# Kernel optimization log

Measured on AMD Instinct MI355X. Metric: run time of the kernel, lower is better.

The kernel has to match this reference:

```python
import jax, jax.numpy as jnp
import numpy as np

B, N, D = 256, 133, 1024
H, C = 8, 128  # per-head channels; H*C == out_channels
NEG_SLOPE = 0.2


def setup_inputs() -> dict:
    key = jax.random.key(0)
    kx, kw, ka, kadj = jax.random.split(key, 4)
    x = jax.random.normal(kx, (B, N, D), dtype=jnp.float32)
    W = jax.random.normal(kw, (H * C, D), dtype=jnp.float32) * 0.02  # nn.Linear weight (out,in)
    attn_w = jax.random.normal(ka, (2 * C,), dtype=jnp.float32) * 0.02  # attn Linear(2C,1) weight
    # binary adjacency with self-loops so every softmax column has a valid entry
    bern = (jax.random.uniform(kadj, (N, N)) < 0.15).astype(jnp.float32)
    adj = jnp.maximum(bern, jnp.eye(N, dtype=jnp.float32))[:, :, None]  # (N,N,1)
    return {"x": x, "W": W, "attn_w": attn_w, "adj": adj}


def reference(x, W, attn_w, adj):
    b, n, _ = x.shape
    g = (x @ W.T).reshape(b, n, H, C)  # (B,N,H,C)
    # concat(g_j, g_i) @ attn_w == g_j @ wl + g_i @ wr (leakyrelu applied after the sum)
    wl, wr = attn_w[:C], attn_w[C:]
    sj = jnp.einsum('bnhc,c->bnh', g, wl)  # score contribution from g[b, j]
    si = jnp.einsum('bnhc,c->bnh', g, wr)  # score contribution from g[b, i]
    e = jax.nn.leaky_relu(si[:, :, None, :] + sj[:, None, :, :], NEG_SLOPE)  # (B,N,N,H) e[b,i,j,h]
    e = jnp.where(adj[None] == 0, -jnp.inf, e)
    a = jax.nn.softmax(e, axis=1)  # faithful to original: softmax over dim=1 (the i axis)
    # dropout omitted (inference/eval mode)
    out = jnp.einsum('bijh,bjhf->bihf', a, g)  # aggregate over j
    return out.reshape(b, n, H * C)  # is_concat=True
```

## Files before the change

### kernel.cpp

```cpp
#include <hip/hip_runtime.h>

#define NB    133
#define NBP   136
#define BATCH 256
#define HEADS 8
#define CDIM  128
#define DDIM  1024
#define MROWS (BATCH * NB)
#define NDIM  (HEADS * CDIM)
#define BH    (BATCH * HEADS)
#define NT    32

typedef __bf16 bf16_t;
typedef bf16_t bf16x8 __attribute__((ext_vector_type(8)));
typedef float  f32x4  __attribute__((ext_vector_type(4)));

__device__ __forceinline__ unsigned short f2bf(float f) {
  unsigned u = __float_as_uint(f);
  u += 0x7fffu + ((u >> 16) & 1u);
  return (unsigned short)(u >> 16);
}
__device__ __forceinline__ void load_lds16(const void* g, void* l) {
  __builtin_amdgcn_global_load_lds(
      (__attribute__((address_space(1))) void*)(g),
      (__attribute__((address_space(3))) void*)(l), 16, 0, 0);
}
__device__ __forceinline__ void bar() {
  asm volatile("" ::: "memory");
  __builtin_amdgcn_s_barrier();
  asm volatile("" ::: "memory");
}
#define VMWAIT(n) asm volatile("s_waitcnt vmcnt(" #n ")" ::: "memory")

__global__ __launch_bounds__(256) void cvt_kernel(const float* __restrict__ x,
                                                  const float* __restrict__ W,
                                                  unsigned short* __restrict__ xb,
                                                  unsigned short* __restrict__ wb) {
  const int nx = MROWS * DDIM / 8, nw = NDIM * DDIM / 8;
  int i = blockIdx.x * 256 + threadIdx.x;
  const float* src; unsigned short* dst; int k;
  if (i < nx)           { src = x; dst = xb; k = i; }
  else if (i < nx + nw) { src = W; dst = wb; k = i - nx; }
  else return;
  const float4* s4 = (const float4*)src;
  float4 a = s4[(size_t)k * 2];
  float4 b = s4[(size_t)k * 2 + 1];
  union { unsigned short u[8]; uint4 v; } p;
  p.u[0] = f2bf(a.x); p.u[1] = f2bf(a.y); p.u[2] = f2bf(a.z); p.u[3] = f2bf(a.w);
  p.u[4] = f2bf(b.x); p.u[5] = f2bf(b.y); p.u[6] = f2bf(b.z); p.u[7] = f2bf(b.w);
  ((uint4*)dst)[k] = p.v;
}

__global__ __launch_bounds__(192) void mask_kernel(const float* __restrict__ adj,
                                                   unsigned* __restrict__ rm,
                                                   unsigned* __restrict__ cm) {
  const int tid = threadIdx.x, lane = tid & 63, wv = tid >> 6, blk = blockIdx.x;
  if (blk < 144) {
    const int i = blk;
    bool on = (i < NB) && (tid < NB) && (adj[i * NB + tid] != 0.f);
    unsigned long long bb = __ballot(on);
    if (lane == 0)  rm[i * 6 + wv * 2]     = (unsigned)bb;
    if (lane == 32) rm[i * 6 + wv * 2 + 1] = (unsigned)(bb >> 32);
  } else {
    const int j = blk - 144;
    bool on = (tid < NB) && (adj[tid * NB + j] != 0.f);
    unsigned long long bb = __ballot(on);
    if (lane == 0)  cm[j * 6 + wv * 2]     = (unsigned)bb;
    if (lane == 32) cm[j * 6 + wv * 2 + 1] = (unsigned)(bb >> 32);
  }
}

__global__ __launch_bounds__(512, 2) void gemm_kernel(const unsigned short* __restrict__ xb,
                                                      const unsigned short* __restrict__ wb,
                                                      const float* __restrict__ attn_w,
                                                      unsigned short* __restrict__ gb,
                                                      float* __restrict__ si_ws,
                                                      float* __restrict__ sj_ws) {
  __shared__ __attribute__((aligned(16))) unsigned short lds[4][2][8192];
  __shared__ float sred[2][8][128];

  const int tid = threadIdx.x;
  const int bn = blockIdx.x & 3, bm = blockIdx.x >> 2;
  const int lane = tid & 63, w = tid >> 6;
  const int wr = w >> 2, wc = w & 3;
  const int q = lane >> 4, li = lane & 15;
  const int sub = (q ^ ((li >> 1) & 3)) * 8;

  const unsigned short* Ab = xb + (size_t)bm * 256 * DDIM;
  const unsigned short* Bb = wb + (size_t)bn * 256 * DDIM;

  const int u0 = tid, u1 = tid + 512;
  const size_t sa0 = (size_t)(u0 >> 2) * DDIM + (((u0 & 3) ^ ((u0 >> 3) & 3)) * 8);
  const size_t sa1 = (size_t)(u1 >> 2) * DDIM + (((u1 & 3) ^ ((u1 >> 3) & 3)) * 8);

  f32x4 acc[8][4] = {};

#define STAGE(T) do { \
    unsigned short* _la = &lds[(T) & 3][0][0]; \
    unsigned short* _lb = &lds[(T) & 3][1][0]; \
    const int _k = (T) * 32; \
    load_lds16(Ab + sa0 + _k, _la + u0 * 8); \
    load_lds16(Ab + sa1 + _k, _la + u1 * 8); \
    load_lds16(Bb + sa0 + _k, _lb + u0 * 8); \
    load_lds16(Bb + sa1 + _k, _lb + u1 * 8); \
  } while (0)

#define COMPUTE(T) do { \
    const unsigned short* _as = &lds[(T) & 3][0][0]; \
    const unsigned short* _bs = &lds[(T) & 3][1][0]; \
    bf16x8 af[8], bfr[4]; \
    _Pragma("unroll") \
    for (int mi = 0; mi < 8; ++mi) \
      af[mi] = *(const bf16x8*)&_as[(wr * 128 + mi * 16 + li) * 32 + sub]; \
    _Pragma("unroll") \
    for (int ni = 0; ni < 4; ++ni) \
      bfr[ni] = *(const bf16x8*)&_bs[(wc * 64 + ni * 16 + li) * 32 + sub]; \
    __builtin_amdgcn_s_setprio(1); \
    _Pragma("unroll") \
    for (int mi = 0; mi < 8; ++mi) \
      _Pragma("unroll") \
      for (int ni = 0; ni < 4; ++ni) \
        acc[mi][ni] = __builtin_amdgcn_mfma_f32_16x16x32_bf16(af[mi], bfr[ni], acc[mi][ni], 0, 0, 0); \
    __builtin_amdgcn_s_setprio(0); \
  } while (0)

  STAGE(0); STAGE(1); STAGE(2);
  VMWAIT(8);
  bar();
  for (int t = 0; t < NT - 3; ++t) {
    STAGE(t + 3);
    COMPUTE(t);
    VMWAIT(8);
    bar();
  }
  COMPUTE(NT - 3); VMWAIT(4); bar();
  COMPUTE(NT - 2); VMWAIT(0); bar();
  COMPUTE(NT - 1);

  float wlv[4], wrv[4];
#pragma unroll
  for (int ni = 0; ni < 4; ++ni) {
    const int cc = (wc & 1) * 64 + ni * 16 + li;
    wlv[ni] = attn_w[cc];
    wrv[ni] = attn_w[CDIM + cc];
  }
#pragma unroll
  for (int mi = 0; mi < 8; ++mi)
#pragma unroll
    for (int rr = 0; rr < 4; ++rr) {
      float pj = 0.f, pi = 0.f;
#pragma unroll
      for (int ni = 0; ni < 4; ++ni) {
        pj += acc[mi][ni][rr] * wlv[ni];
        pi += acc[mi][ni][rr] * wrv[ni];
      }
#pragma unroll
      for (int d = 1; d < 16; d <<= 1) {
        pj += __shfl_xor(pj, d);
        pi += __shfl_xor(pi, d);
      }
      if (li == 0) {
        sred[0][w][mi * 16 + q * 4 + rr] = pj;
        sred[1][w][mi * 16 + q * 4 + rr] = pi;
      }
    }
  __syncthreads();
#pragma unroll
  for (int idx0 = 0; idx0 < 2; ++idx0) {
    const int idx = idx0 * 512 + tid;
    const int row = idx & 255;
    const int hw = (idx >> 8) & 1;
    const int which = idx >> 9;
    const int wb2 = (row >> 7) * 4 + hw * 2;
    const float v = sred[which][wb2][row & 127] + sred[which][wb2 + 1][row & 127];
    const int rg = bm * 256 + row;
    const int b = rg / NB, n = rg - b * NB;
    const int h = bn * 2 + hw;
    float* dst = which ? si_ws : sj_ws;
    dst[(b * HEADS + h) * NB + n] = v;
  }

#pragma unroll
  for (int mi = 0; mi < 8; ++mi)
#pragma unroll
    for (int ni = 0; ni < 4; ++ni) {
      const int col = bn * 256 + wc * 64 + ni * 16 + li;
      const size_t row0 = (size_t)(bm * 256 + wr * 128 + mi * 16 + q * 4);
#pragma unroll
      for (int rr = 0; rr < 4; ++rr)
        gb[(row0 + rr) * NDIM + col] = f2bf(acc[mi][ni][rr]);
    }
#undef STAGE
#undef COMPUTE
}

__global__ __launch_bounds__(192) void stats_kernel(const float* __restrict__ si_ws,
                                                    const float* __restrict__ sj_ws,
                                                    const unsigned* __restrict__ cm,
                                                    float2* __restrict__ smrg) {
  __shared__ float siL[NB];
  const int tid = threadIdx.x;
  const int base = blockIdx.x * NB;
  if (tid < NB) siL[tid] = si_ws[base + tid];
  __syncthreads();
  if (tid >= 160) return;
  float2 o = {0.f, 0.f};
  if (tid < NB) {
    const int j = tid;
    const float sjv = sj_ws[base + j];
    float m = -3.0e38f;
#pragma unroll
    for (int wd = 0; wd < 5; ++wd) {
      unsigned bits = cm[j * 6 + wd];
      while (bits) {
        const int i = __ffs(bits) - 1; bits &= bits - 1;
        float e = siL[wd * 32 + i] + sjv;
        e = e > 0.f ? e : 0.2f * e;
        m = fmaxf(m, e);
      }
    }
    float s = 0.f;
#pragma unroll
    for (int wd = 0; wd < 5; ++wd) {
      unsigned bits = cm[j * 6 + wd];
      while (bits) {
        const int i = __ffs(bits) - 1; bits &= bits - 1;
        float e = siL[wd * 32 + i] + sjv;
        e = e > 0.f ? e : 0.2f * e;
        s += __expf(e - m);
      }
    }
    o.x = sjv;
    o.y = m + __logf(s);
  }
  smrg[(size_t)blockIdx.x * 160 + tid] = o;
}

__global__ __launch_bounds__(256) void agg_kernel(const unsigned short* __restrict__ gb,
                                                  const float* __restrict__ si_ws,
                                                  const float2* __restrict__ smrg,
                                                  const unsigned* __restrict__ rm,
                                                  float* __restrict__ out) {
  __shared__ __attribute__((aligned(16))) unsigned short gTl[64 * NBP + 32];
  __shared__ __attribute__((aligned(8))) float2 smrL[160];
  const int tid = threadIdx.x;
  const int bh = blockIdx.x >> 1, fh = blockIdx.x & 1;
  const int b = bh >> 3, h = bh & 7;
  const int base = bh * NB;

  if (tid < 64) {
    gTl[tid * NBP + 133] = 0;
    *(unsigned*)&gTl[tid * NBP + 134] = 0;
  }
  if (tid >= 64 && tid < 80) *(unsigned*)&gTl[64 * NBP + 2 * (tid - 64)] = 0;
  if (tid < 160) smrL[tid] = smrg[(size_t)bh * 160 + tid];

  const unsigned short* gsrc = gb + (size_t)(b * NB) * NDIM + h * CDIM + fh * 64;
  for (int u = tid; u < NB * 16; u += 256) {
    const int j = u >> 4, fg = u & 15;
    const uint2 d = *(const uint2*)(gsrc + (size_t)j * NDIM + fg * 4);
    const int f0 = fg * 4;
    gTl[(f0 + 0) * NBP + j] = (unsigned short)(d.x);
    gTl[(f0 + 1) * NBP + j] = (unsigned short)(d.x >> 16);
    gTl[(f0 + 2) * NBP + j] = (unsigned short)(d.y);
    gTl[(f0 + 3) * NBP + j] = (unsigned short)(d.y >> 16);
  }
  __syncthreads();

  const int lane = tid & 63, wv = tid >> 6, q = lane >> 4, li = lane & 15;
  for (int mt = wv; mt < 9; mt += 4) {
    const int il = mt * 16 + li;
    const float si_r = si_ws[base + (il < NB ? il : NB - 1)];
    const unsigned* rmr = rm + il * 6;
    f32x4 acc[4] = {};
#pragma unroll
    for (int ks = 0; ks < 5; ++ks) {
      const int j0 = ks * 32 + q * 8;
      const unsigned bits = rmr[ks] >> (q * 8);
      bf16x8 afv;
#pragma unroll
      for (int jj = 0; jj < 8; ++jj) {
        const float2 sv = smrL[j0 + jj];
        float e = si_r + sv.x;
        e = e > 0.f ? e : 0.2f * e;
        const float wgt = ((bits >> jj) & 1u) ? __expf(e - sv.y) : 0.f;
        afv[jj] = (bf16_t)wgt;
      }
#pragma unroll
      for (int n = 0; n < 4; ++n) {
        const bf16x8 bv = *(const bf16x8*)&gTl[(n * 16 + li) * NBP + j0];
        acc[n] = __builtin_amdgcn_mfma_f32_16x16x32_bf16(afv, bv, acc[n], 0, 0, 0);
      }
    }
    float* obase = out + (size_t)(b * NB) * NDIM + h * CDIM + fh * 64;
#pragma unroll
    for (int n = 0; n < 4; ++n)
#pragma unroll
      for (int rr = 0; rr < 4; ++rr) {
        const int i = mt * 16 + q * 4 + rr;
        if (i < NB) obase[(size_t)i * NDIM + n * 16 + li] = acc[n][rr];
      }
  }
}

extern "C" void kernel_launch(void* const* d_in, const int* in_sizes, int n_in,
                              void* d_out, int out_size, void* d_ws, size_t ws_size,
                              hipStream_t stream) {
  const float* x      = (const float*)d_in[0];
  const float* W      = (const float*)d_in[1];
  const float* attn_w = (const float*)d_in[2];
  const float* adj    = (const float*)d_in[3];
  float* out = (float*)d_out;
  char* ws = (char*)d_ws;

  unsigned short* xb = (unsigned short*)(ws + 0);
  unsigned short* wb = (unsigned short*)(ws + 69730304);
  unsigned short* gb = (unsigned short*)(ws + 71827456);
  float* si = (float*)(ws + 141557760);
  float* sj = (float*)(ws + 142647296);
  unsigned* rm = (unsigned*)(ws + 143736832);
  unsigned* cm = (unsigned*)(ws + 143740288);
  float2* smrg = (float2*)(ws + 0);

  const int ncvt = (MROWS * DDIM + NDIM * DDIM) / 8;
  cvt_kernel<<<(ncvt + 255) / 256, 256, 0, stream>>>(x, W, xb, wb);
  mask_kernel<<<277, 192, 0, stream>>>(adj, rm, cm);
  gemm_kernel<<<133 * 4, 512, 0, stream>>>(xb, wb, attn_w, gb, si, sj);
  stats_kernel<<<BH, 192, 0, stream>>>(si, sj, cm, smrg);
  agg_kernel<<<BH * 2, 256, 0, stream>>>(gb, si, smrg, rm, out);
}
```

Baseline: 472.0 us.

## Restructure GEMM main loop to K=64 double-buffered tiles with interleaved quadrant MFMAs

The projection GEMM moves from four LDS stages of K=32 to two stages of K=64. The compute loop is split into four sub-quadrant MFMA phases, and the next tile's global-to-LDS loads are issued between those phases, so loads, LDS reads and MFMAs overlap more finely. It also remaps block IDs so consecutive tiles land on the same XCD for better L2 locality, and changes the LDS swizzle to an 8-slot XOR. The trade-off is many more barriers per iteration and only a two-deep prefetch, which exposes more load latency.

After: 445.1 us. 1.06x faster.

```diff
diff --git a/kernel.cpp b/kernel.cpp
--- a/kernel.cpp
+++ b/kernel.cpp
@@ -9,7 +9,7 @@
 #define MROWS (BATCH * NB)
 #define NDIM  (HEADS * CDIM)
 #define BH    (BATCH * HEADS)
-#define NT    32
+#define NKT   16
 
 typedef __bf16 bf16_t;
 typedef bf16_t bf16x8 __attribute__((ext_vector_type(8)));
@@ -76,83 +76,120 @@
                                                       unsigned short* __restrict__ gb,
                                                       float* __restrict__ si_ws,
                                                       float* __restrict__ sj_ws) {
-  __shared__ __attribute__((aligned(16))) unsigned short lds[4][2][8192];
+  __shared__ __attribute__((aligned(16))) unsigned short lds[2][2][256 * 64];
   __shared__ float sred[2][8][128];
 
   const int tid = threadIdx.x;
-  const int bn = blockIdx.x & 3, bm = blockIdx.x >> 2;
+  const int orig = blockIdx.x;
+  const int xcd = orig & 7, lo = orig >> 3;
+  const int wg = (xcd < 4) ? (xcd * 67 + lo) : (268 + (xcd - 4) * 66 + lo);
+  const int bn = wg & 3, bm = wg >> 2;
+
   const int lane = tid & 63, w = tid >> 6;
   const int wr = w >> 2, wc = w & 3;
   const int q = lane >> 4, li = lane & 15;
-  const int sub = (q ^ ((li >> 1) & 3)) * 8;
 
   const unsigned short* Ab = xb + (size_t)bm * 256 * DDIM;
   const unsigned short* Bb = wb + (size_t)bn * 256 * DDIM;
 
-  const int u0 = tid, u1 = tid + 512;
-  const size_t sa0 = (size_t)(u0 >> 2) * DDIM + (((u0 & 3) ^ ((u0 >> 3) & 3)) * 8);
-  const size_t sa1 = (size_t)(u1 >> 2) * DDIM + (((u1 & 3) ^ ((u1 >> 3) & 3)) * 8);
-
-  f32x4 acc[8][4] = {};
-
-#define STAGE(T) do { \
-    unsigned short* _la = &lds[(T) & 3][0][0]; \
-    unsigned short* _lb = &lds[(T) & 3][1][0]; \
-    const int _k = (T) * 32; \
-    load_lds16(Ab + sa0 + _k, _la + u0 * 8); \
-    load_lds16(Ab + sa1 + _k, _la + u1 * 8); \
-    load_lds16(Bb + sa0 + _k, _lb + u0 * 8); \
-    load_lds16(Bb + sa1 + _k, _lb + u1 * 8); \
+  int soff[4];
+#pragma unroll
+  for (int i = 0; i < 4; ++i) {
+    const int f = tid + i * 512;
+    const int row = f >> 3, slot = f & 7;
+    soff[i] = row * DDIM + ((slot ^ (row & 7)) << 3);
+  }
+#define STG(gp_, buf_, kt_, h_) do { \
+    load_lds16((gp_) + soff[(h_) * 2]     + (kt_) * 64, (buf_) + (tid + (h_) * 1024) * 8); \
+    load_lds16((gp_) + soff[(h_) * 2 + 1] + (kt_) * 64, (buf_) + (tid + 512 + (h_) * 1024) * 8); \
   } while (0)
 
-#define COMPUTE(T) do { \
-    const unsigned short* _as = &lds[(T) & 3][0][0]; \
-    const unsigned short* _bs = &lds[(T) & 3][1][0]; \
-    bf16x8 af[8], bfr[4]; \
-    _Pragma("unroll") \
-    for (int mi = 0; mi < 8; ++mi) \
-      af[mi] = *(const bf16x8*)&_as[(wr * 128 + mi * 16 + li) * 32 + sub]; \
-    _Pragma("unroll") \
-    for (int ni = 0; ni < 4; ++ni) \
-      bfr[ni] = *(const bf16x8*)&_bs[(wc * 64 + ni * 16 + li) * 32 + sub]; \
-    __builtin_amdgcn_s_setprio(1); \
-    _Pragma("unroll") \
-    for (int mi = 0; mi < 8; ++mi) \
-      _Pragma("unroll") \
-      for (int ni = 0; ni < 4; ++ni) \
-        acc[mi][ni] = __builtin_amdgcn_mfma_f32_16x16x32_bf16(af[mi], bfr[ni], acc[mi][ni], 0, 0, 0); \
-    __builtin_amdgcn_s_setprio(0); \
-  } while (0)
-
-  STAGE(0); STAGE(1); STAGE(2);
+  const int sl0 = ((q ^ (li & 7)) << 3);
+  const int sl1 = (((4 + q) ^ (li & 7)) << 3);
+  const int arow = (wr * 128 + li) * 64;
+  const int brow = (wc * 64 + li) * 64;
+
+  f32x4 acc[2][2][4][2] = {};
+  bf16x8 a[4][2], b0f[2][2], b1f[2][2];
+
+  {
+    unsigned short* A0 = &lds[0][0][0]; unsigned short* B0 = &lds[0][1][0];
+    unsigned short* A1 = &lds[1][0][0]; unsigned short* B1 = &lds[1][1][0];
+    STG(Bb, B0, 0, 0); STG(Bb, B0, 0, 1); STG(Ab, A0, 0, 0); STG(Ab, A0, 0, 1);
+    STG(Bb, B1, 1, 0); STG(Bb, B1, 1, 1); STG(Ab, A1, 1, 0); STG(Ab, A1, 1, 1);
+  }
   VMWAIT(8);
   bar();
-  for (int t = 0; t < NT - 3; ++t) {
-    STAGE(t + 3);
-    COMPUTE(t);
-    VMWAIT(8);
-    bar();
-  }
-  COMPUTE(NT - 3); VMWAIT(4); bar();
-  COMPUTE(NT - 2); VMWAIT(0); bar();
-  COMPUTE(NT - 1);
+
+#define LDA(mq_) { _Pragma("unroll") for (int mi = 0; mi < 4; ++mi) { \
+      const int r_ = arow + ((mq_) * 64 + mi * 16) * 64; \
+      a[mi][0] = *(const bf16x8*)&as[r_ + sl0]; \
+      a[mi][1] = *(const bf16x8*)&as[r_ + sl1]; } }
+#define LDB(dst_, nq_) { _Pragma("unroll") for (int ni = 0; ni < 2; ++ni) { \
+      const int r_ = brow + ((nq_) * 32 + ni * 16) * 64; \
+      dst_[ni][0] = *(const bf16x8*)&bs[r_ + sl0]; \
+      dst_[ni][1] = *(const bf16x8*)&bs[r_ + sl1]; } }
+#define MM(mq_, nq_, bv_) { \
+      __builtin_amdgcn_s_setprio(1); \
+      _Pragma("unroll") for (int mi = 0; mi < 4; ++mi) \
+      _Pragma("unroll") for (int ni = 0; ni < 2; ++ni) { \
+        acc[mq_][nq_][mi][ni] = __builtin_amdgcn_mfma_f32_16x16x32_bf16(a[mi][0], bv_[ni][0], acc[mq_][nq_][mi][ni], 0, 0, 0); \
+        acc[mq_][nq_][mi][ni] = __builtin_amdgcn_mfma_f32_16x16x32_bf16(a[mi][1], bv_[ni][1], acc[mq_][nq_][mi][ni], 0, 0, 0); } \
+      __builtin_amdgcn_s_setprio(0); }
+
+#pragma unroll 2
+  for (int t = 0; t < NKT; ++t) {
+    const unsigned short* as = &lds[t & 1][0][0];
+    const unsigned short* bs = &lds[t & 1][1][0];
+    unsigned short* asw = &lds[t & 1][0][0];
+    unsigned short* bsw = &lds[t & 1][1][0];
+
+    LDA(0); LDB(b0f, 0);
+    bar();
+    MM(0, 0, b0f);
+    bar();
+    LDB(b1f, 1);
+    bar();
+    MM(0, 1, b1f);
+    bar();
+    LDA(1);
+    if (t < NKT - 2) { STG(Bb, bsw, t + 2, 0); STG(Bb, bsw, t + 2, 1); }
+    bar();
+    MM(1, 1, b1f);
+    bar();
+    if (t < NKT - 2) {
+      STG(Ab, asw, t + 2, 0); STG(Ab, asw, t + 2, 1);
+      VMWAIT(8);
+    } else {
+      VMWAIT(0);
+    }
+    bar();
+    MM(1, 0, b0f);
+    bar();
+  }
+#undef LDA
+#undef LDB
+#undef MM
+#undef STG
+
+#define ACC(m8, n4) acc[(m8) >> 2][(n4) >> 1][(m8) & 3][(n4) & 1]
 
   float wlv[4], wrv[4];
 #pragma unroll
-  for (int ni = 0; ni < 4; ++ni) {
-    const int cc = (wc & 1) * 64 + ni * 16 + li;
-    wlv[ni] = attn_w[cc];
-    wrv[ni] = attn_w[CDIM + cc];
-  }
-#pragma unroll
-  for (int mi = 0; mi < 8; ++mi)
+  for (int n4 = 0; n4 < 4; ++n4) {
+    const int cc = (wc & 1) * 64 + n4 * 16 + li;
+    wlv[n4] = attn_w[cc];
+    wrv[n4] = attn_w[CDIM + cc];
+  }
+#pragma unroll
+  for (int m8 = 0; m8 < 8; ++m8)
 #pragma unroll
     for (int rr = 0; rr < 4; ++rr) {
       float pj = 0.f, pi = 0.f;
 #pragma unroll
-      for (int ni = 0; ni < 4; ++ni) {
-        pj += acc[mi][ni][rr] * wlv[ni];
-        pi += acc[mi][ni][rr] * wrv[ni];
+      for (int n4 = 0; n4 < 4; ++n4) {
+        pj += ACC(m8, n4)[rr] * wlv[n4];
+        pi += ACC(m8, n4)[rr] * wrv[n4];
       }
 #pragma unroll
       for (int d = 1; d < 16; d <<= 1) {
@@ -160,8 +197,8 @@
         pi += __shfl_xor(pi, d);
       }
       if (li == 0) {
-        sred[0][w][mi * 16 + q * 4 + rr] = pj;
-        sred[1][w][mi * 16 + q * 4 + rr] = pi;
+        sred[0][w][m8 * 16 + q * 4 + rr] = pj;
+        sred[1][w][m8 * 16 + q * 4 + rr] = pi;
       }
     }
   __syncthreads();
@@ -181,17 +218,16 @@
   }
 
 #pragma unroll
-  for (int mi = 0; mi < 8; ++mi)
-#pragma unroll
-    for (int ni = 0; ni < 4; ++ni) {
-      const int col = bn * 256 + wc * 64 + ni * 16 + li;
-      const size_t row0 = (size_t)(bm * 256 + wr * 128 + mi * 16 + q * 4);
+  for (int m8 = 0; m8 < 8; ++m8)
+#pragma unroll
+    for (int n4 = 0; n4 < 4; ++n4) {
+      const int col = bn * 256 + wc * 64 + n4 * 16 + li;
+      const size_t row0 = (size_t)(bm * 256 + wr * 128 + m8 * 16 + q * 4);
 #pragma unroll
       for (int rr = 0; rr < 4; ++rr)
-        gb[(row0 + rr) * NDIM + col] = f2bf(acc[mi][ni][rr]);
-    }
-#undef STAGE
-#undef COMPUTE
+        gb[(row0 + rr) * NDIM + col] = f2bf(ACC(m8, n4)[rr]);
+    }
+#undef ACC
 }
 
 __global__ __launch_bounds__(192) void stats_kernel(const float* __restrict__ si_ws,
```
